# Kernel optimization log

Hardware: AMD Instinct MI355X
Metric: run time of the kernel (lower is better)

## Reference

```python
import jax, jax.numpy as jnp
import numpy as np

B, L, D, H1, OUT, MAX_W = 16, 128, 768, 770, 40, 30


def _span_mask():
    # valid spans: i <= j and width < MAX_W (structured sparsity over the L x L grid)
    ii, jj = np.meshgrid(np.arange(L), np.arange(L), indexing='ij')
    return ((jj >= ii) & (jj - ii < MAX_W)).astype(np.int32)


def setup_inputs():
    key = jax.random.key(0)
    ks = jax.random.split(key, 5)
    hidden_states = jax.random.normal(ks[0], (B, L + 1, D), dtype=jnp.float32)
    rng = np.random.default_rng(0)
    starts = rng.integers(0, L - MAX_W, size=(B,))
    ends = starts + rng.integers(0, MAX_W, size=(B,))
    pred_spans = jnp.asarray(np.stack([starts, ends], axis=1), dtype=jnp.int32)
    span_mask = jnp.asarray(_span_mask())
    W1 = 0.02 * jax.random.normal(ks[1], (2 * D + 1, H1), dtype=jnp.float32)
    b1 = jax.random.normal(ks[2], (H1,), dtype=jnp.float32)
    W2 = 0.02 * jax.random.normal(ks[3], (H1, OUT), dtype=jnp.float32)
    b2 = jax.random.normal(ks[4], (OUT,), dtype=jnp.float32)
    return dict(hidden_states=hidden_states, pred_spans=pred_spans, token_num=L,
                span_available_indication_matrix=span_mask,
                W1=W1, b1=b1, W2=W2, b2=b2)


def reference(hidden_states, pred_spans, token_num, span_available_indication_matrix, W1, b1, W2, b2):
    # span mask is an integer constant -> resolve valid (i, j) pairs on host
    mask = np.asarray(span_available_indication_matrix)
    vi, vj = np.nonzero(mask == 1)            # [n_valid] each
    vi_j = jnp.asarray(vi)
    vj_j = jnp.asarray(vj)
    vecs = hidden_states[:, 1:token_num + 1, :]  # token t -> hidden[:, t+1, :], [B, L, D]
    xi = vecs[:, vi_j, :]                        # [B, n_valid, D] gather of span-start vecs
    xj = vecs[:, vj_j, :]                        # [B, n_valid, D] gather of span-end vecs
    # pred_indications: 2 if span == pred span; 1 if strictly inside it (i<=j); else 0
    s = pred_spans[:, 0:1]
    e = pred_spans[:, 1:2]
    i_ = vi_j[None, :]
    j_ = vj_j[None, :]
    exact = (i_ == s) & (j_ == e)
    inside = (i_ >= s) & (j_ <= e) & (i_ <= j_)
    ind = jnp.where(exact, 2.0, jnp.where(inside, 1.0, 0.0)).astype(hidden_states.dtype)  # [B, n_valid]
    # Linear over concat([xi, xj, ind]) expressed as split matmuls (avoids materializing concat)
    W1i, W1j, w1c = W1[:D], W1[D:2 * D], W1[2 * D]
    h = (jnp.einsum('bnd,dh->bnh', xi, W1i)
         + jnp.einsum('bnd,dh->bnh', xj, W1j)
         + ind[..., None] * w1c + b1)
    h = jax.nn.relu(h)
    logits = jnp.einsum('bnh,ho->bno', h, W2) + b2   # [B, n_valid, OUT]
    return jax.nn.log_softmax(logits, axis=-1)
```

## Files before the change

kernel.cpp:

```cpp
#include <hip/hip_runtime.h>
#include <math.h>

#define B_ 16
#define L_ 128
#define D_ 768
#define H1_ 770
#define OUT_ 40
#define NPAIRS 3405
#define NLOG 1540
#define YSB 1552
#define VOFFB 776
#define KPAD 800
#define NPAD 48
#define W2T_S 800
#define W1TROWS 1600

typedef __attribute__((ext_vector_type(8))) short bf16x8;
typedef __attribute__((ext_vector_type(8))) unsigned short u16x8;
typedef __attribute__((ext_vector_type(4))) float f32x4;
typedef __attribute__((ext_vector_type(4))) unsigned int u32x4;

__device__ inline unsigned short f2bf(float f) {
  unsigned int u = __builtin_bit_cast(unsigned int, f);
  u += 0x7fffu + ((u >> 16) & 1u);
  return (unsigned short)(u >> 16);
}
__device__ inline float bf2f(unsigned short x) {
  return __builtin_bit_cast(float, (unsigned int)x << 16);
}

#if __has_builtin(__builtin_amdgcn_cvt_pk_bf16_f32)
typedef __attribute__((ext_vector_type(2))) __bf16 bf16x2_t;
__device__ inline unsigned int pack_bf16(float lo, float hi) {
  bf16x2_t r = __builtin_amdgcn_cvt_pk_bf16_f32(lo, hi);
  return __builtin_bit_cast(unsigned int, r);
}
#else
__device__ inline unsigned int pack_bf16(float lo, float hi) {
  return (unsigned int)f2bf(lo) | ((unsigned int)f2bf(hi) << 16);
}
#endif

typedef const __attribute__((address_space(1))) void* gas_t;
typedef __attribute__((address_space(3))) void* las_t;
__device__ inline void gl2lds16(const void* g, void* l) {
  __builtin_amdgcn_global_load_lds((gas_t)g, (las_t)l, 16, 0, 0);
}

#define XCVT_N (2048 * 192)

__global__ __launch_bounds__(256) void prep_all(
    const float* __restrict__ hidden, const float* __restrict__ W1,
    const float* __restrict__ b1, const float* __restrict__ W2,
    unsigned short* __restrict__ Xb, unsigned short* __restrict__ W2T,
    float* __restrict__ Cv)
{
  int idx = blockIdx.x * 256 + threadIdx.x;
  if (idx < XCVT_N) {
    int m = idx / 192;
    int c = idx - m * 192;
    float4 f = *(const float4*)(hidden + (size_t)(m + (m >> 7) + 1) * D_ + c * 4);
    ushort4 o;
    o.x = f2bf(f.x); o.y = f2bf(f.y); o.z = f2bf(f.z); o.w = f2bf(f.w);
    *(ushort4*)(Xb + (size_t)m * D_ + c * 4) = o;
    return;
  }
  idx -= XCVT_N;
  const float* w1c = W1 + 1536 * H1_;
  if (idx < NPAD * KPAD) {
    int n = idx / KPAD, k = idx - n * KPAD;
    float v = (n < OUT_ && k < H1_) ? W2[k * OUT_ + n] : 0.f;
    W2T[idx] = f2bf(v);
  } else if (idx < NPAD * KPAD + 3 * KPAD) {
    int c = idx - NPAD * KPAD;
    int t = c / KPAD, k = c - t * KPAD;
    Cv[c] = (k < H1_) ? (b1[k] + (float)t * w1c[k]) : 0.f;
  }
}

__global__ __launch_bounds__(256) void w1t_kernel(
    const float* __restrict__ W1, unsigned short* __restrict__ W1T)
{
  __shared__ float t[32][33];
  const int tx = threadIdx.x & 31, ty = threadIdx.x >> 5;
  const int n0 = blockIdx.x * 32, k0 = blockIdx.y * 32;
  #pragma unroll
  for (int r = 0; r < 4; ++r) {
    int k = k0 + ty + r * 8, n = n0 + tx;
    float v = 0.f;
    if (n < H1_)       v = W1[k * H1_ + n];
    else if (n < NLOG) v = W1[(D_ + k) * H1_ + (n - H1_)];
    t[ty + r * 8][tx] = v;
  }
  __syncthreads();
  #pragma unroll
  for (int r = 0; r < 4; ++r) {
    int n = n0 + ty + r * 8, k = k0 + tx;
    W1T[(size_t)n * D_ + k] = f2bf(t[tx][ty + r * 8]);
  }
}

__global__ __launch_bounds__(256) void gemm1_mfma(
    const unsigned short* __restrict__ Xb, const unsigned short* __restrict__ W1T,
    unsigned short* __restrict__ Yb)
{
  __shared__ unsigned short As[64][64];
  __shared__ unsigned short Bs[64][64];
  const int tid = threadIdx.x;
  const int lane = tid & 63, w = tid >> 6;
  const int lm = lane & 15, q = lane >> 4;
  const int row0 = blockIdx.y * 64, col0 = blockIdx.x * 64;
  const int m0 = (w >> 1) * 32, n0 = (w & 1) * 32;

  const int srow = w * 16 + (lane >> 3);
  const int schunk = (lane & 7) * 8;
  const unsigned short* ga = Xb  + (size_t)(row0 + srow) * D_ + schunk;
  const unsigned short* gb = W1T + (size_t)(col0 + srow) * D_ + schunk;
  unsigned short* la = &As[w * 16][0];
  unsigned short* lb = &Bs[w * 16][0];

  f32x4 acc[2][2] = {};

  for (int k0 = 0; k0 < D_; k0 += 64) {
    gl2lds16(ga + k0,           la);
    gl2lds16(ga + k0 + 8 * D_,  la + 8 * 64);
    gl2lds16(gb + k0,           lb);
    gl2lds16(gb + k0 + 8 * D_,  lb + 8 * 64);
    __syncthreads();

    #pragma unroll
    for (int ks = 0; ks < 2; ++ks) {
      bf16x8 a0 = *(const bf16x8*)&As[m0 + lm]     [ks * 32 + q * 8];
      bf16x8 a1 = *(const bf16x8*)&As[m0 + 16 + lm][ks * 32 + q * 8];
      bf16x8 b0 = *(const bf16x8*)&Bs[n0 + lm]     [ks * 32 + q * 8];
      bf16x8 b1 = *(const bf16x8*)&Bs[n0 + 16 + lm][ks * 32 + q * 8];
      acc[0][0] = __builtin_amdgcn_mfma_f32_16x16x32_bf16(a0, b0, acc[0][0], 0, 0, 0);
      acc[0][1] = __builtin_amdgcn_mfma_f32_16x16x32_bf16(a0, b1, acc[0][1], 0, 0, 0);
      acc[1][0] = __builtin_amdgcn_mfma_f32_16x16x32_bf16(a1, b0, acc[1][0], 0, 0, 0);
      acc[1][1] = __builtin_amdgcn_mfma_f32_16x16x32_bf16(a1, b1, acc[1][1], 0, 0, 0);
    }
    __syncthreads();
  }

  #pragma unroll
  for (int ti = 0; ti < 2; ++ti) {
    #pragma unroll
    for (int tj = 0; tj < 2; ++tj) {
      int col = col0 + n0 + tj * 16 + lm;
      if (col >= NLOG) continue;
      int pc = (col < H1_) ? col : col + (VOFFB - H1_);
      #pragma unroll
      for (int r = 0; r < 4; ++r) {
        int row = row0 + m0 + ti * 16 + q * 4 + r;
        Yb[(size_t)row * YSB + pc] = f2bf(acc[ti][tj][r]);
      }
    }
  }
}

__device__ inline void pair_ij(int n, int& i, int& j) {
  if (n < 2970) {
    i = n / 30;
    j = i + (n - i * 30);
  } else {
    int m = n - 2970;
    int r = 0, w = 29;
    while (m >= w) { m -= w; --w; ++r; }
    i = 99 + r;
    j = i + m;
  }
}

__global__ __launch_bounds__(256) void pair_mfma(
    const unsigned short* __restrict__ Yb, const int* __restrict__ spans,
    const unsigned short* __restrict__ W2T, const float* __restrict__ Cv,
    const float* __restrict__ b2, float* __restrict__ out)
{
  const int tid = threadIdx.x;
  const int bb = blockIdx.y;
  const int pair0 = blockIdx.x * 64;
  const int lane = tid & 63, w = tid >> 6;
  const int lm = lane & 15, q = lane >> 4;

  int apair = pair0 + w * 16 + lm;
  int ai = 0, aj = 0;
  if (apair < NPAIRS) pair_ij(apair, ai, aj);
  const int s = spans[2 * bb], e = spans[2 * bb + 1];
  const int ind = (ai == s && aj == e) ? 2 : ((ai >= s && aj <= e) ? 1 : 0);

  const unsigned short* uptr = Yb + (size_t)(bb * L_ + ai) * YSB + q * 8;
  const unsigned short* vptr = Yb + (size_t)(bb * L_ + aj) * YSB + VOFFB + q * 8;
  const float* cptr = Cv + ind * KPAD + q * 8;
  const unsigned short* bp0 = W2T + (0 * 16 + lm) * W2T_S + q * 8;
  const unsigned short* bp1 = W2T + (1 * 16 + lm) * W2T_S + q * 8;
  const unsigned short* bp2 = W2T + (2 * 16 + lm) * W2T_S + q * 8;

  f32x4 acc0 = {}, acc1 = {}, acc2 = {};

  #pragma unroll 5
  for (int ks = 0; ks < 25; ++ks) {
    const int ko = ks * 32;
    u16x8 uu = *(const u16x8*)(uptr + ko);
    u16x8 vv = *(const u16x8*)(vptr + ko);
    float4 c0 = *(const float4*)(cptr + ko);
    float4 c1 = *(const float4*)(cptr + ko + 4);
    float h0 = fmaxf(bf2f(uu[0]) + bf2f(vv[0]) + c0.x, 0.f);
    float h1 = fmaxf(bf2f(uu[1]) + bf2f(vv[1]) + c0.y, 0.f);
    float h2 = fmaxf(bf2f(uu[2]) + bf2f(vv[2]) + c0.z, 0.f);
    float h3 = fmaxf(bf2f(uu[3]) + bf2f(vv[3]) + c0.w, 0.f);
    float h4 = fmaxf(bf2f(uu[4]) + bf2f(vv[4]) + c1.x, 0.f);
    float h5 = fmaxf(bf2f(uu[5]) + bf2f(vv[5]) + c1.y, 0.f);
    float h6 = fmaxf(bf2f(uu[6]) + bf2f(vv[6]) + c1.z, 0.f);
    float h7 = fmaxf(bf2f(uu[7]) + bf2f(vv[7]) + c1.w, 0.f);
    u32x4 hp;
    hp[0] = pack_bf16(h0, h1);
    hp[1] = pack_bf16(h2, h3);
    hp[2] = pack_bf16(h4, h5);
    hp[3] = pack_bf16(h6, h7);
    bf16x8 a = __builtin_bit_cast(bf16x8, hp);
    bf16x8 bf0 = *(const bf16x8*)(bp0 + ko);
    bf16x8 bf1 = *(const bf16x8*)(bp1 + ko);
    bf16x8 bf2v = *(const bf16x8*)(bp2 + ko);
    acc0 = __builtin_amdgcn_mfma_f32_16x16x32_bf16(a, bf0, acc0, 0, 0, 0);
    acc1 = __builtin_amdgcn_mfma_f32_16x16x32_bf16(a, bf1, acc1, 0, 0, 0);
    acc2 = __builtin_amdgcn_mfma_f32_16x16x32_bf16(a, bf2v, acc2, 0, 0, 0);
  }

  const float b2v0 = b2[lm];
  const float b2v1 = b2[16 + lm];
  const float b2v2 = (lm < 8) ? b2[32 + lm] : 0.f;

  #pragma unroll
  for (int r = 0; r < 4; ++r) {
    float l0 = acc0[r] + b2v0;
    float l1 = acc1[r] + b2v1;
    float l2 = (lm < 8) ? (acc2[r] + b2v2) : -INFINITY;
    float mx = fmaxf(fmaxf(l0, l1), l2);
    mx = fmaxf(mx, __shfl_xor(mx, 1));
    mx = fmaxf(mx, __shfl_xor(mx, 2));
    mx = fmaxf(mx, __shfl_xor(mx, 4));
    mx = fmaxf(mx, __shfl_xor(mx, 8));
    float sm = expf(l0 - mx) + expf(l1 - mx) + ((lm < 8) ? expf(l2 - mx) : 0.f);
    sm += __shfl_xor(sm, 1);
    sm += __shfl_xor(sm, 2);
    sm += __shfl_xor(sm, 4);
    sm += __shfl_xor(sm, 8);
    float lsd = mx + logf(sm);

    int pair = pair0 + w * 16 + q * 4 + r;
    if (pair < NPAIRS) {
      float* op = out + ((size_t)bb * NPAIRS + pair) * OUT_;
      op[lm]      = l0 - lsd;
      op[16 + lm] = l1 - lsd;
      if (lm < 8) op[32 + lm] = l2 - lsd;
    }
  }
}

extern "C" void kernel_launch(void* const* d_in, const int* in_sizes, int n_in,
                              void* d_out, int out_size, void* d_ws, size_t ws_size,
                              hipStream_t stream) {
  const float* hidden = (const float*)d_in[0];
  const int*   spans  = (const int*)d_in[1];
  const float* W1 = (const float*)d_in[4];
  const float* b1 = (const float*)d_in[5];
  const float* W2 = (const float*)d_in[6];
  const float* b2 = (const float*)d_in[7];
  float* out = (float*)d_out;

  char* base = (char*)d_ws;
  size_t off = 0;
  auto take = [&](size_t bytes) {
    char* p = base + off;
    off = (off + bytes + 255) & ~(size_t)255;
    return p;
  };
  unsigned short* Yb  = (unsigned short*)take((size_t)2049 * YSB * 2);
  unsigned short* Xb  = (unsigned short*)take((size_t)2048 * D_ * 2);
  unsigned short* W1T = (unsigned short*)take((size_t)W1TROWS * D_ * 2);
  unsigned short* W2T = (unsigned short*)take((size_t)NPAD * KPAD * 2);
  float*          Cv  = (float*)take((size_t)3 * KPAD * 4);

  prep_all<<<dim3((XCVT_N + NPAD * KPAD + 3 * KPAD + 255) / 256), 256, 0, stream>>>(
      hidden, W1, b1, W2, Xb, W2T, Cv);
  w1t_kernel<<<dim3(50, 24), 256, 0, stream>>>(W1, W1T);
  gemm1_mfma<<<dim3(25, 32), 256, 0, stream>>>(Xb, W1T, Yb);
  pair_mfma<<<dim3((NPAIRS + 63) / 64, B_), 256, 0, stream>>>(
      Yb, spans, W2T, Cv, b2, out);
}
```

Before: 134.1 us.

## Merge prep kernels, double-buffer GEMM1, tile pair kernel by 4x4 span blocks

Folds the W1 transpose into the single prep launch, removing one kernel launch. GEMM1 now double-buffers its LDS tiles so the next K-slice loads while the current one computes, and it drops one barrier per iteration. The pair kernel groups pairs into 4x4 (i,j) tiles so each wave reuses a few Yb rows, and it reads W2 pre-swizzled into the MFMA fragment layout for coalesced loads. The cost is padded work on partially valid tiles and extra masking when writing outputs.

```diff
diff --git a/kernel.cpp b/kernel.cpp
--- a/kernel.cpp
+++ b/kernel.cpp
@@ -12,8 +12,9 @@
 #define VOFFB 776
 #define KPAD 800
 #define NPAD 48
-#define W2T_S 800
 #define W1TROWS 1600
+#define NTILES 252
+#define NKS 25
 
 typedef __attribute__((ext_vector_type(8))) short bf16x8;
 typedef __attribute__((ext_vector_type(8))) unsigned short u16x8;
@@ -47,16 +48,22 @@
   __builtin_amdgcn_global_load_lds((gas_t)g, (las_t)l, 16, 0, 0);
 }
 
-#define XCVT_N (2048 * 192)
+#define NB_X 1536
+#define NB_W 160
+#define NB_T 1200
 
 __global__ __launch_bounds__(256) void prep_all(
     const float* __restrict__ hidden, const float* __restrict__ W1,
     const float* __restrict__ b1, const float* __restrict__ W2,
-    unsigned short* __restrict__ Xb, unsigned short* __restrict__ W2T,
-    float* __restrict__ Cv)
+    unsigned short* __restrict__ Xb, unsigned short* __restrict__ W1T,
+    unsigned short* __restrict__ Bswz, float* __restrict__ Cv)
 {
-  int idx = blockIdx.x * 256 + threadIdx.x;
-  if (idx < XCVT_N) {
+  __shared__ float t[32][33];
+  int bx = blockIdx.x;
+  const int tid = threadIdx.x;
+
+  if (bx < NB_X) {
+    int idx = bx * 256 + tid;
     int m = idx / 192;
     int c = idx - m * 192;
     float4 f = *(const float4*)(hidden + (size_t)(m + (m >> 7) + 1) * D_ + c * 4);
@@ -65,25 +72,30 @@
     *(ushort4*)(Xb + (size_t)m * D_ + c * 4) = o;
     return;
   }
-  idx -= XCVT_N;
-  const float* w1c = W1 + 1536 * H1_;
-  if (idx < NPAD * KPAD) {
-    int n = idx / KPAD, k = idx - n * KPAD;
-    float v = (n < OUT_ && k < H1_) ? W2[k * OUT_ + n] : 0.f;
-    W2T[idx] = f2bf(v);
-  } else if (idx < NPAD * KPAD + 3 * KPAD) {
-    int c = idx - NPAD * KPAD;
-    int t = c / KPAD, k = c - t * KPAD;
-    Cv[c] = (k < H1_) ? (b1[k] + (float)t * w1c[k]) : 0.f;
-  }
-}
-
-__global__ __launch_bounds__(256) void w1t_kernel(
-    const float* __restrict__ W1, unsigned short* __restrict__ W1T)
-{
-  __shared__ float t[32][33];
-  const int tx = threadIdx.x & 31, ty = threadIdx.x >> 5;
-  const int n0 = blockIdx.x * 32, k0 = blockIdx.y * 32;
+  bx -= NB_X;
+  if (bx < NB_W) {
+    int idx = bx * 256 + tid;
+    if (idx < NKS * 3 * 512) {
+      int ks = idx / 1536;
+      int rem = idx - ks * 1536;
+      int f = rem / 512;
+      int l = (rem - f * 512) >> 3;
+      int e = rem & 7;
+      int n = f * 16 + (l & 15);
+      int k = ks * 32 + (l >> 4) * 8 + e;
+      float v = (n < OUT_ && k < H1_) ? W2[k * OUT_ + n] : 0.f;
+      Bswz[idx] = f2bf(v);
+    } else if (idx < NKS * 3 * 512 + 3 * KPAD) {
+      int c = idx - NKS * 3 * 512;
+      int tt = c / KPAD, k = c - tt * KPAD;
+      const float* w1c = W1 + 1536 * H1_;
+      Cv[c] = (k < H1_) ? (b1[k] + (float)tt * w1c[k]) : 0.f;
+    }
+    return;
+  }
+  bx -= NB_W;
+  const int tx = tid & 31, ty = tid >> 5;
+  const int n0 = (bx % 50) * 32, k0 = (bx / 50) * 32;
   #pragma unroll
   for (int r = 0; r < 4; ++r) {
     int k = k0 + ty + r * 8, n = n0 + tx;
@@ -104,8 +116,8 @@
     const unsigned short* __restrict__ Xb, const unsigned short* __restrict__ W1T,
     unsigned short* __restrict__ Yb)
 {
-  __shared__ unsigned short As[64][64];
-  __shared__ unsigned short Bs[64][64];
+  __shared__ unsigned short As[2][64][64];
+  __shared__ unsigned short Bs[2][64][64];
   const int tid = threadIdx.x;
   const int lane = tid & 63, w = tid >> 6;
   const int lm = lane & 15, q = lane >> 4;
@@ -116,30 +128,32 @@
   const int schunk = (lane & 7) * 8;
   const unsigned short* ga = Xb  + (size_t)(row0 + srow) * D_ + schunk;
   const unsigned short* gb = W1T + (size_t)(col0 + srow) * D_ + schunk;
-  unsigned short* la = &As[w * 16][0];
-  unsigned short* lb = &Bs[w * 16][0];
 
   f32x4 acc[2][2] = {};
 
-  for (int k0 = 0; k0 < D_; k0 += 64) {
-    gl2lds16(ga + k0,           la);
-    gl2lds16(ga + k0 + 8 * D_,  la + 8 * 64);
-    gl2lds16(gb + k0,           lb);
-    gl2lds16(gb + k0 + 8 * D_,  lb + 8 * 64);
+  auto stage = [&](int k0, int b) {
+    gl2lds16(ga + k0,          &As[b][w * 16][0]);
+    gl2lds16(ga + k0 + 8 * D_, &As[b][w * 16 + 8][0]);
+    gl2lds16(gb + k0,          &Bs[b][w * 16][0]);
+    gl2lds16(gb + k0 + 8 * D_, &Bs[b][w * 16 + 8][0]);
+  };
+
+  stage(0, 0);
+  for (int it = 0; it < 12; ++it) {
+    const int cur = it & 1;
     __syncthreads();
-
+    if (it < 11) stage((it + 1) * 64, cur ^ 1);
     #pragma unroll
     for (int ks = 0; ks < 2; ++ks) {
-      bf16x8 a0 = *(const bf16x8*)&As[m0 + lm]     [ks * 32 + q * 8];
-      bf16x8 a1 = *(const bf16x8*)&As[m0 + 16 + lm][ks * 32 + q * 8];
-      bf16x8 b0 = *(const bf16x8*)&Bs[n0 + lm]     [ks * 32 + q * 8];
-      bf16x8 b1 = *(const bf16x8*)&Bs[n0 + 16 + lm][ks * 32 + q * 8];
+      bf16x8 a0 = *(const bf16x8*)&As[cur][m0 + lm]     [ks * 32 + q * 8];
+      bf16x8 a1 = *(const bf16x8*)&As[cur][m0 + 16 + lm][ks * 32 + q * 8];
+      bf16x8 b0 = *(const bf16x8*)&Bs[cur][n0 + lm]     [ks * 32 + q * 8];
+      bf16x8 b1 = *(const bf16x8*)&Bs[cur][n0 + 16 + lm][ks * 32 + q * 8];
       acc[0][0] = __builtin_amdgcn_mfma_f32_16x16x32_bf16(a0, b0, acc[0][0], 0, 0, 0);
       acc[0][1] = __builtin_amdgcn_mfma_f32_16x16x32_bf16(a0, b1, acc[0][1], 0, 0, 0);
       acc[1][0] = __builtin_amdgcn_mfma_f32_16x16x32_bf16(a1, b0, acc[1][0], 0, 0, 0);
       acc[1][1] = __builtin_amdgcn_mfma_f32_16x16x32_bf16(a1, b1, acc[1][1], 0, 0, 0);
     }
-    __syncthreads();
   }
 
   #pragma unroll
@@ -158,47 +172,47 @@
   }
 }
 
-__device__ inline void pair_ij(int n, int& i, int& j) {
-  if (n < 2970) {
-    i = n / 30;
-    j = i + (n - i * 30);
-  } else {
-    int m = n - 2970;
-    int r = 0, w = 29;
+__device__ inline void tile_decode(int T, int& ti, int& d) {
+  if (T < 216) { ti = T / 9; d = T - ti * 9; }
+  else {
+    int m = T - 216; int r = 24, w = 8;
     while (m >= w) { m -= w; --w; ++r; }
-    i = 99 + r;
-    j = i + m;
-  }
+    ti = r; d = m;
+  }
+}
+__device__ inline int pair_rank(int i, int j) {
+  return (i < 99) ? i * 30 + (j - i)
+                  : NPAIRS - (128 - i) * (129 - i) / 2 + (j - i);
 }
 
 __global__ __launch_bounds__(256) void pair_mfma(
     const unsigned short* __restrict__ Yb, const int* __restrict__ spans,
-    const unsigned short* __restrict__ W2T, const float* __restrict__ Cv,
+    const unsigned short* __restrict__ Bswz, const float* __restrict__ Cv,
     const float* __restrict__ b2, float* __restrict__ out)
 {
   const int tid = threadIdx.x;
   const int bb = blockIdx.y;
-  const int pair0 = blockIdx.x * 64;
   const int lane = tid & 63, w = tid >> 6;
   const int lm = lane & 15, q = lane >> 4;
 
-  int apair = pair0 + w * 16 + lm;
-  int ai = 0, aj = 0;
-  if (apair < NPAIRS) pair_ij(apair, ai, aj);
+  int ti, d;
+  tile_decode(blockIdx.x * 4 + w, ti, d);
+  const int i0 = ti * 4, j0 = (ti + d) * 4;
+
+  const int ai = i0 + (lm & 3);
+  const int aj = j0 + (lm >> 2);
   const int s = spans[2 * bb], e = spans[2 * bb + 1];
   const int ind = (ai == s && aj == e) ? 2 : ((ai >= s && aj <= e) ? 1 : 0);
 
   const unsigned short* uptr = Yb + (size_t)(bb * L_ + ai) * YSB + q * 8;
   const unsigned short* vptr = Yb + (size_t)(bb * L_ + aj) * YSB + VOFFB + q * 8;
   const float* cptr = Cv + ind * KPAD + q * 8;
-  const unsigned short* bp0 = W2T + (0 * 16 + lm) * W2T_S + q * 8;
-  const unsigned short* bp1 = W2T + (1 * 16 + lm) * W2T_S + q * 8;
-  const unsigned short* bp2 = W2T + (2 * 16 + lm) * W2T_S + q * 8;
+  const unsigned short* bbase = Bswz + lane * 8;
 
   f32x4 acc0 = {}, acc1 = {}, acc2 = {};
 
   #pragma unroll 5
-  for (int ks = 0; ks < 25; ++ks) {
+  for (int ks = 0; ks < NKS; ++ks) {
     const int ko = ks * 32;
     u16x8 uu = *(const u16x8*)(uptr + ko);
     u16x8 vv = *(const u16x8*)(vptr + ko);
@@ -218,9 +232,9 @@
     hp[2] = pack_bf16(h4, h5);
     hp[3] = pack_bf16(h6, h7);
     bf16x8 a = __builtin_bit_cast(bf16x8, hp);
-    bf16x8 bf0 = *(const bf16x8*)(bp0 + ko);
-    bf16x8 bf1 = *(const bf16x8*)(bp1 + ko);
-    bf16x8 bf2v = *(const bf16x8*)(bp2 + ko);
+    bf16x8 bf0 = *(const bf16x8*)(bbase + (size_t)(ks * 3 + 0) * 512);
+    bf16x8 bf1 = *(const bf16x8*)(bbase + (size_t)(ks * 3 + 1) * 512);
+    bf16x8 bf2v = *(const bf16x8*)(bbase + (size_t)(ks * 3 + 2) * 512);
     acc0 = __builtin_amdgcn_mfma_f32_16x16x32_bf16(a, bf0, acc0, 0, 0, 0);
     acc1 = __builtin_amdgcn_mfma_f32_16x16x32_bf16(a, bf1, acc1, 0, 0, 0);
     acc2 = __builtin_amdgcn_mfma_f32_16x16x32_bf16(a, bf2v, acc2, 0, 0, 0);
@@ -229,6 +243,7 @@
   const float b2v0 = b2[lm];
   const float b2v1 = b2[16 + lm];
   const float b2v2 = (lm < 8) ? b2[32 + lm] : 0.f;
+  const int oi = i0 , oj = j0 + q;
 
   #pragma unroll
   for (int r = 0; r < 4; ++r) {
@@ -247,9 +262,9 @@
     sm += __shfl_xor(sm, 8);
     float lsd = mx + logf(sm);
 
-    int pair = pair0 + w * 16 + q * 4 + r;
-    if (pair < NPAIRS) {
-      float* op = out + ((size_t)bb * NPAIRS + pair) * OUT_;
+    int pi_ = oi + r, pj_ = oj;
+    if (pj_ >= pi_ && (pj_ - pi_) < 30) {
+      float* op = out + ((size_t)bb * NPAIRS + pair_rank(pi_, pj_)) * OUT_;
       op[lm]      = l0 - lsd;
       op[16 + lm] = l1 - lsd;
       if (lm < 8) op[32 + lm] = l2 - lsd;
@@ -275,16 +290,14 @@
     off = (off + bytes + 255) & ~(size_t)255;
     return p;
   };
-  unsigned short* Yb  = (unsigned short*)take((size_t)2049 * YSB * 2);
-  unsigned short* Xb  = (unsigned short*)take((size_t)2048 * D_ * 2);
-  unsigned short* W1T = (unsigned short*)take((size_t)W1TROWS * D_ * 2);
-  unsigned short* W2T = (unsigned short*)take((size_t)NPAD * KPAD * 2);
-  float*          Cv  = (float*)take((size_t)3 * KPAD * 4);
-
-  prep_all<<<dim3((XCVT_N + NPAD * KPAD + 3 * KPAD + 255) / 256), 256, 0, stream>>>(
-      hidden, W1, b1, W2, Xb, W2T, Cv);
-  w1t_kernel<<<dim3(50, 24), 256, 0, stream>>>(W1, W1T);
+  unsigned short* Yb   = (unsigned short*)take((size_t)2049 * YSB * 2);
+  unsigned short* Xb   = (unsigned short*)take((size_t)2048 * D_ * 2);
+  unsigned short* W1T  = (unsigned short*)take((size_t)W1TROWS * D_ * 2);
+  unsigned short* Bswz = (unsigned short*)take((size_t)NKS * 3 * 512 * 2);
+  float*          Cv   = (float*)take((size_t)3 * KPAD * 4);
+
+  prep_all<<<dim3(NB_X + NB_W + NB_T), 256, 0, stream>>>(
+      hidden, W1, b1, W2, Xb, W1T, Bswz, Cv);
   gemm1_mfma<<<dim3(25, 32), 256, 0, stream>>>(Xb, W1T, Yb);
-  pair_mfma<<<dim3((NPAIRS + 63) / 64, B_), 256, 0, stream>>>(
-      Yb, spans, W2T, Cv, b2, out);
-}
+  pair_mfma<<<dim3(63, B_), 256, 0, stream>>>(Yb, spans, Bswz, Cv, b2, out);
+}
```

Result: no change. 135.1 us (+0.7%).
